# Kernel tuning notes

Measured on AMD Instinct MI355X. Metric: run time of the kernel, lower is better.

Reference implementation:

```python
import jax, jax.numpy as jnp
import numpy as np

EMBED_DIM = 768
NUM_HEADS = 12
EPS = 1e-6


def setup_inputs() -> dict:
    key = jax.random.key(0)
    ks = jax.random.split(key, 9)
    B, C, H, W = 8, EMBED_DIM, 48, 48
    std = 0.02
    E = EMBED_DIM
    return {
        "query": jax.random.normal(ks[0], (B, C, H, W), dtype=jnp.float32),
        "Wq": jax.random.normal(ks[1], (E, E), dtype=jnp.float32) * std,
        "bq": jnp.zeros((E,), dtype=jnp.float32),
        "Wk": jax.random.normal(ks[2], (E, E), dtype=jnp.float32) * std,
        "bk": jnp.zeros((E,), dtype=jnp.float32),
        "Wv": jax.random.normal(ks[3], (E, E), dtype=jnp.float32) * std,
        "bv": jnp.zeros((E,), dtype=jnp.float32),
        "Wo": jax.random.normal(ks[4], (E, E), dtype=jnp.float32) * std,
        "bo": jnp.zeros((E,), dtype=jnp.float32),
    }


def reference(query, Wq, bq, Wk, bk, Wv, bv, Wo, bo):
    # query: (B, C, H, W) -> (L, B, E) with L = H*W
    B, C, H, W = query.shape
    L = H * W
    E = C
    h = NUM_HEADS
    d = E // h
    x = query.reshape(B, C, L).transpose(2, 0, 1)  # (L, B, E)

    # cos/sin positional reweighting: pi/2 * (i+1) / L
    idx = (jnp.pi / 2) * jnp.arange(1, L + 1, dtype=x.dtype) / L
    sin = jnp.sin(idx)[None, :, None]  # (1, L, 1)
    cos = jnp.cos(idx)[None, :, None]

    # projections + relu feature map
    q = jax.nn.relu(x @ Wq.T + bq)
    k = jax.nn.relu(x @ Wk.T + bk)
    v = x @ Wv.T + bv

    def to_heads(t):  # (L, B, E) -> (B*h, L, d)
        return t.reshape(L, B * h, d).transpose(1, 0, 2)

    q, k, v = to_heads(q), to_heads(k), to_heads(v)

    q_ = jnp.concatenate([q * sin, q * cos], axis=-1)  # (n, L, 2d)
    k_ = jnp.concatenate([k * sin, k * cos], axis=-1)

    # non-causal linear attention
    kv = jnp.einsum("nld,nlm->ndm", k_, v)              # (n, 2d, d)
    z = 1.0 / jnp.maximum(jnp.einsum("nld,nd->nl", q_, k_.sum(axis=1)), EPS)
    out = jnp.einsum("nld,ndm,nl->nlm", q_, kv, z)       # (n, L, d)

    # residual (DropPath is identity at inference)
    attn = x + out.transpose(1, 0, 2).reshape(L, B, E)
    return attn @ Wo.T + bo
```

## Files before the change

### kernel.cpp

```cpp
#include <hip/hip_runtime.h>


#define L_SEQ 2304
#define BATCH 8
#define EDIM 768
#define NHEAD 12
#define DHEAD 64
#define MROWS (L_SEQ * BATCH)

typedef __attribute__((ext_vector_type(8))) short bf16x8_t;
typedef __attribute__((ext_vector_type(4))) float f32x4_t;

__device__ __forceinline__ float b2f(unsigned short u) {
  union { unsigned int i; float f; } x; x.i = ((unsigned int)u) << 16; return x.f;
}
__device__ __forceinline__ unsigned short f2b(float f) {
  union { float f; unsigned int i; } x; x.f = f;
  unsigned int r = x.i + 0x7FFFu + ((x.i >> 16) & 1u);
  return (unsigned short)(r >> 16);
}

#define GLOAD_LDS16(g, l)                                                     \
  __builtin_amdgcn_global_load_lds(                                           \
      (const __attribute__((address_space(1))) unsigned int*)(g),             \
      (__attribute__((address_space(3))) unsigned int*)(l), 16, 0, 0)

__global__ __launch_bounds__(256) void conv_w(
    const float* __restrict__ W0, const float* __restrict__ W1,
    const float* __restrict__ W2, const float* __restrict__ W3,
    unsigned short* __restrict__ dst) {
  const float* W = (blockIdx.y == 0) ? W0 : (blockIdx.y == 1) ? W1
                 : (blockIdx.y == 2) ? W2 : W3;
  unsigned short* d = dst + (size_t)blockIdx.y * EDIM * EDIM;
  int idx = blockIdx.x * 256 + threadIdx.x;
  float4 v = *(const float4*)(W + (size_t)idx * 4);
  ushort4 o;
  o.x = f2b(v.x); o.y = f2b(v.y); o.z = f2b(v.z); o.w = f2b(v.w);
  *(ushort4*)(d + (size_t)idx * 4) = o;
}

__global__ __launch_bounds__(256) void transpose_q(
    const float* __restrict__ q, unsigned short* __restrict__ xT) {
  __shared__ float tile[64][65];
  int b = blockIdx.z;
  int e0 = blockIdx.x * 64;
  int l0 = blockIdx.y * 64;
  int t = threadIdx.x;
  int li = t & 63, er = t >> 6;
#pragma unroll
  for (int p = 0; p < 16; p++) {
    int eo = er + p * 4;
    tile[eo][li] = q[((size_t)b * EDIM + (e0 + eo)) * L_SEQ + (l0 + li)];
  }
  __syncthreads();
  int ei = t & 63, lr = t >> 6;
#pragma unroll
  for (int p = 0; p < 16; p++) {
    int lo = lr + p * 4;
    xT[((size_t)b * L_SEQ + (l0 + lo)) * EDIM + (e0 + ei)] = f2b(tile[ei][lo]);
  }
}

template <int MODE>
__global__ __launch_bounds__(256) void gemm_bt(
    const unsigned short* __restrict__ A,
    const unsigned short* __restrict__ Wall,
    const float* __restrict__ bias0, const float* __restrict__ bias1,
    const float* __restrict__ bias2,
    unsigned short* __restrict__ dst0, unsigned short* __restrict__ dst1,
    unsigned short* __restrict__ dst2,
    float* __restrict__ dstf) {
  constexpr int BM = 128, BN = 128, BK = 32, K = EDIM;
  __shared__ __align__(16) unsigned short As[BM * BK];
  __shared__ __align__(16) unsigned short Bs[BN * BK];

  const unsigned short* W;
  const float* bias;
  unsigned short* dst;
  bool do_relu;
  if (MODE == 0) {
    int z = blockIdx.z;
    W    = Wall + (size_t)z * EDIM * EDIM;
    bias = (z == 0) ? bias0 : (z == 1) ? bias1 : bias2;
    dst  = (z == 0) ? dst0 : (z == 1) ? dst1 : dst2;
    do_relu = (z < 2);
  } else {
    W = Wall; bias = bias0; dst = dst0; do_relu = false;
  }

  int t = threadIdx.x;
  int lane = t & 63;
  int wave = t >> 6;
  int wr = (wave & 1) * 64;
  int wc = (wave >> 1) * 64;
  int row0 = blockIdx.x * BM;
  int col0 = blockIdx.y * BN;
  int mrow = lane & 15, quad = lane >> 4;

  f32x4_t acc[4][4] = {};

  for (int k0 = 0; k0 < K; k0 += BK) {
#pragma unroll
    for (int i = 0; i < 2; i++) {
      int c = t + i * 256;
      int r = c >> 2;
      int kk = (c & 3) * 8;
      GLOAD_LDS16(A + (size_t)(row0 + r) * K + (k0 + kk), As + (size_t)c * 8);
      GLOAD_LDS16(W + (size_t)(col0 + r) * K + (k0 + kk), Bs + (size_t)c * 8);
    }
    __syncthreads();
    bf16x8_t af[4], bfr[4];
#pragma unroll
    for (int i = 0; i < 4; i++) {
      af[i]  = *(const bf16x8_t*)(As + (wr + i * 16 + mrow) * BK + quad * 8);
      bfr[i] = *(const bf16x8_t*)(Bs + (wc + i * 16 + mrow) * BK + quad * 8);
    }
#pragma unroll
    for (int ti = 0; ti < 4; ti++)
#pragma unroll
      for (int tj = 0; tj < 4; tj++)
        acc[ti][tj] = __builtin_amdgcn_mfma_f32_16x16x32_bf16(af[ti], bfr[tj], acc[ti][tj], 0, 0, 0);
    __syncthreads();
  }

  int bb = row0 / L_SEQ;
#pragma unroll
  for (int ti = 0; ti < 4; ti++) {
#pragma unroll
    for (int tj = 0; tj < 4; tj++) {
      int gc = col0 + wc + tj * 16 + (lane & 15);
      float bv = bias[gc];
#pragma unroll
      for (int r = 0; r < 4; r++) {
        int gr = row0 + wr + ti * 16 + quad * 4 + r;
        float v = acc[ti][tj][r] + bv;
        if (MODE == 0) {
          if (do_relu) v = fmaxf(v, 0.0f);
          int ll = gr - bb * L_SEQ;
          int n = bb * NHEAD + (gc >> 6);
          dst[((size_t)n * L_SEQ + ll) * DHEAD + (gc & 63)] = f2b(v);
        } else {
          dstf[(size_t)gr * EDIM + gc] = v;
        }
      }
    }
  }
}

__global__ __launch_bounds__(256) void kv_mfma(
    const unsigned short* __restrict__ kbuf, const unsigned short* __restrict__ vbuf,
    float* __restrict__ kv, float* __restrict__ ksum) {
  constexpr int ST = 40;
  __shared__ __align__(16) unsigned short ksT[128 * ST];
  __shared__ __align__(16) unsigned short vsT[80 * ST];
  int n = blockIdx.x;
  int lbase = blockIdx.y * 288;
  int t = threadIdx.x;
  int lane = t & 63, wave = t >> 6;
  int mrow = lane & 15, quad = lane >> 4;

  for (int i = t; i < 16 * ST; i += 256) {
    int row = i / ST, col = i % ST;
    vsT[(64 + row) * ST + col] = (row == 0 && col < 32) ? (unsigned short)0x3F80 : 0;
  }

  int lrd = t >> 3;
  int oct = t & 7;
  const unsigned short* kbase = kbuf + (size_t)n * L_SEQ * DHEAD + oct * 8;
  const unsigned short* vbase = vbuf + (size_t)n * L_SEQ * DHEAD + oct * 8;

  f32x4_t acc[2][5] = {};

  for (int s = 0; s < 9; s++) {
    int l = lbase + s * 32 + lrd;
    float sv, cv;
    sincosf(1.5707963267948966f * (float)(l + 1) / 2304.0f, &sv, &cv);
    union { uint4 q; unsigned short u[8]; } kq, vq;
    kq.q = *(const uint4*)(kbase + (size_t)l * DHEAD);
    vq.q = *(const uint4*)(vbase + (size_t)l * DHEAD);
    __syncthreads();
#pragma unroll
    for (int e = 0; e < 8; e++) {
      int d = oct * 8 + e;
      float kval = b2f(kq.u[e]);
      ksT[d * ST + lrd] = f2b(kval * sv);
      ksT[(64 + d) * ST + lrd] = f2b(kval * cv);
      vsT[d * ST + lrd] = vq.u[e];
    }
    __syncthreads();
    bf16x8_t af[2];
#pragma unroll
    for (int ti = 0; ti < 2; ti++)
      af[ti] = *(const bf16x8_t*)(ksT + ((wave * 2 + ti) * 16 + mrow) * ST + quad * 8);
#pragma unroll
    for (int tj = 0; tj < 5; tj++) {
      bf16x8_t bfv = *(const bf16x8_t*)(vsT + (tj * 16 + mrow) * ST + quad * 8);
#pragma unroll
      for (int ti = 0; ti < 2; ti++)
        acc[ti][tj] = __builtin_amdgcn_mfma_f32_16x16x32_bf16(af[ti], bfv, acc[ti][tj], 0, 0, 0);
    }
  }

#pragma unroll
  for (int ti = 0; ti < 2; ti++) {
#pragma unroll
    for (int r = 0; r < 4; r++) {
      int j = (wave * 2 + ti) * 16 + quad * 4 + r;
#pragma unroll
      for (int tj = 0; tj < 4; tj++) {
        int m = tj * 16 + mrow;
        atomicAdd(&kv[((size_t)n * 128 + j) * 64 + m], acc[ti][tj][r]);
      }
      if (mrow == 0) atomicAdd(&ksum[n * 128 + j], acc[ti][4][r]);
    }
  }
}

__global__ __launch_bounds__(256) void attn_mfma(
    const unsigned short* __restrict__ qbuf, const float* __restrict__ kv,
    const float* __restrict__ ksum, const unsigned short* __restrict__ xT,
    unsigned short* __restrict__ attn) {
  __shared__ __align__(16) unsigned short As[128 * 72];
  __shared__ __align__(16) unsigned short Bs[64 * 136];
  __shared__ float ks_l[128];
  __shared__ float zs[128], zc[128];
  int l0 = blockIdx.x * 128;
  int n = blockIdx.y;
  int t = threadIdx.x;
  int lane = t & 63, wave = t >> 6;
  int mrow = lane & 15, quad = lane >> 4;
  int b = n / NHEAD, hd = n % NHEAD;

  {
    int row = t >> 1, off = (t & 1) * 32;
    const unsigned short* src = qbuf + ((size_t)n * L_SEQ + l0 + row) * DHEAD + off;
    unsigned short* d = As + row * 72 + off;
#pragma unroll
    for (int c = 0; c < 4; c++)
      *(uint4*)(d + c * 8) = *(const uint4*)(src + c * 8);
  }
  {
    int j = t >> 1, mh = (t & 1) * 32;
    const float* src = kv + ((size_t)n * 128 + j) * 64 + mh;
#pragma unroll
    for (int mm = 0; mm < 32; mm++)
      Bs[(mh + mm) * 136 + j] = f2b(src[mm]);
  }
  if (t < 128) ks_l[t] = ksum[n * 128 + t];
  __syncthreads();

  if (t < 128) {
    float d0 = 0.f, d1 = 0.f;
    const unsigned short* arow = As + t * 72;
#pragma unroll
    for (int j = 0; j < 8; j++) {
      bf16x8_t v = *(const bf16x8_t*)(arow + j * 8);
#pragma unroll
      for (int e = 0; e < 8; e++) {
        float qv = b2f((unsigned short)v[e]);
        d0 += qv * ks_l[j * 8 + e];
        d1 += qv * ks_l[64 + j * 8 + e];
      }
    }
    float sv, cv;
    sincosf(1.5707963267948966f * (float)(l0 + t + 1) / 2304.0f, &sv, &cv);
    float z = 1.0f / fmaxf(sv * d0 + cv * d1, 1e-6f);
    zs[t] = z * sv;
    zc[t] = z * cv;
  }
  __syncthreads();

  int wr = wave * 32;
  f32x4_t acc0[2][4] = {}, acc1[2][4] = {};
#pragma unroll
  for (int ks = 0; ks < 2; ks++) {
    bf16x8_t af[2];
#pragma unroll
    for (int ti = 0; ti < 2; ti++)
      af[ti] = *(const bf16x8_t*)(As + (wr + ti * 16 + mrow) * 72 + ks * 32 + quad * 8);
#pragma unroll
    for (int tj = 0; tj < 4; tj++) {
      bf16x8_t b0 = *(const bf16x8_t*)(Bs + (tj * 16 + mrow) * 136 + ks * 32 + quad * 8);
      bf16x8_t b1 = *(const bf16x8_t*)(Bs + (tj * 16 + mrow) * 136 + 64 + ks * 32 + quad * 8);
#pragma unroll
      for (int ti = 0; ti < 2; ti++) {
        acc0[ti][tj] = __builtin_amdgcn_mfma_f32_16x16x32_bf16(af[ti], b0, acc0[ti][tj], 0, 0, 0);
        acc1[ti][tj] = __builtin_amdgcn_mfma_f32_16x16x32_bf16(af[ti], b1, acc1[ti][tj], 0, 0, 0);
      }
    }
  }

#pragma unroll
  for (int ti = 0; ti < 2; ti++) {
#pragma unroll
    for (int tj = 0; tj < 4; tj++) {
      int m = tj * 16 + mrow;
#pragma unroll
      for (int r = 0; r < 4; r++) {
        int row = wr + ti * 16 + quad * 4 + r;
        int l = l0 + row;
        float ov = zs[row] * acc0[ti][tj][r] + zc[row] * acc1[ti][tj][r];
        float xv = b2f(xT[((size_t)b * L_SEQ + l) * EDIM + hd * DHEAD + m]);
        attn[((size_t)l * BATCH + b) * EDIM + hd * DHEAD + m] = f2b(xv + ov);
      }
    }
  }
}

extern "C" void kernel_launch(void* const* d_in, const int* in_sizes, int n_in,
                              void* d_out, int out_size, void* d_ws, size_t ws_size,
                              hipStream_t stream) {
  const float* query = (const float*)d_in[0];
  const float* Wq = (const float*)d_in[1];
  const float* bq = (const float*)d_in[2];
  const float* Wk = (const float*)d_in[3];
  const float* bk = (const float*)d_in[4];
  const float* Wv = (const float*)d_in[5];
  const float* bv = (const float*)d_in[6];
  const float* Wo = (const float*)d_in[7];
  const float* bo = (const float*)d_in[8];
  float* out = (float*)d_out;

  unsigned short* xT = (unsigned short*)d_out;

  char* ws = (char*)d_ws;
  const size_t SZ = (size_t)MROWS * EDIM * 2;
  unsigned short* qbuf = (unsigned short*)(ws);
  unsigned short* kbuf = (unsigned short*)(ws + SZ);
  unsigned short* vbuf = (unsigned short*)(ws + 2 * SZ);
  unsigned short* attn = kbuf;
  float* kv   = (float*)(ws + 3 * SZ);
  float* ksum = (float*)(ws + 3 * SZ + 3145728);
  unsigned short* wbf = (unsigned short*)(ws + 3 * SZ + 3145728 + 49152);

  conv_w<<<dim3(576, 4), 256, 0, stream>>>(Wq, Wk, Wv, Wo, wbf);

  transpose_q<<<dim3(12, 36, 8), 256, 0, stream>>>(query, xT);

  gemm_bt<0><<<dim3(MROWS / 128, EDIM / 128, 3), 256, 0, stream>>>(
      xT, wbf, bq, bk, bv, qbuf, kbuf, vbuf, nullptr);

  hipMemsetAsync(ws + 3 * SZ, 0, 3145728 + 49152, stream);

  kv_mfma<<<dim3(96, 8), 256, 0, stream>>>(kbuf, vbuf, kv, ksum);

  attn_mfma<<<dim3(L_SEQ / 128, 96), 256, 0, stream>>>(qbuf, kv, ksum, xT, attn);

  gemm_bt<1><<<dim3(MROWS / 128, EDIM / 128, 1), 256, 0, stream>>>(
      attn, wbf + 3 * (size_t)EDIM * EDIM, bo, nullptr, nullptr,
      nullptr, nullptr, nullptr, out);
}
```

Before: 329.7 us.

## Replace 128x128 GEMM with pipelined 256x256 tile kernel using swizzled LDS

Replaces the simple 128x128 single-buffered GEMM with a 256x256-tile, 512-thread kernel. It double-buffers K=64 tiles in 128KB of dynamic LDS and loads directly from global into LDS with an XOR swizzle to avoid bank conflicts. Loads are interleaved with MFMA quadrants using explicit barriers, waitcnts and setprio. It also remaps workgroup IDs for XCD-aware locality. The aim is to hide global-load latency and raise MFMA utilisation for the QKV and output projections. In exchange, the grid is much smaller (648 and 216 blocks) with heavier per-block register and LDS use, which limits occupancy and may cause tail effects.

```diff
diff --git a/kernel.cpp b/kernel.cpp
--- a/kernel.cpp
+++ b/kernel.cpp
@@ -61,8 +61,59 @@
   }
 }
 
+#define ALDSO(b_, h_) ((b_) * 16384 + (h_) * 8192)
+#define BLDSO(b_, h_) (32768 + (b_) * 16384 + (h_) * 8192)
+
+#define BARF()                                  \
+  {                                             \
+    asm volatile("" ::: "memory");              \
+    __builtin_amdgcn_s_barrier();               \
+    asm volatile("" ::: "memory");              \
+    __builtin_amdgcn_sched_barrier(0);          \
+  }
+#define WAITL()                                              \
+  {                                                          \
+    asm volatile("s_waitcnt lgkmcnt(0)" ::: "memory");       \
+    __builtin_amdgcn_sched_barrier(0);                       \
+  }
+#define VMW(N) asm volatile("s_waitcnt vmcnt(" #N ")" ::: "memory")
+
+#define STG_A(h_, kt_, LB_)                                                          \
+  {                                                                                  \
+    GLOAD_LDS16(a_sb + (size_t)((h_) * 128) * EDIM + (kt_) * 64, lds + (LB_) + t * 8); \
+    GLOAD_LDS16(a_sb + (size_t)((h_) * 128 + 64) * EDIM + (kt_) * 64,                \
+                lds + (LB_) + 4096 + t * 8);                                         \
+  }
+#define STG_B(h_, kt_, LB_)                                                          \
+  {                                                                                  \
+    GLOAD_LDS16(b_sb + (size_t)((h_) * 128) * EDIM + (kt_) * 64, lds + (LB_) + t * 8); \
+    GLOAD_LDS16(b_sb + (size_t)((h_) * 128 + 64) * EDIM + (kt_) * 64,                \
+                lds + (LB_) + 4096 + t * 8);                                         \
+  }
+
+#define DS_A(SET, B_, H_)                                                            \
+  _Pragma("unroll") for (int i_ = 0; i_ < 4; i_++)                                   \
+  _Pragma("unroll") for (int kk_ = 0; kk_ < 2; kk_++)                                \
+    SET[i_][kk_] = *(const bf16x8_t*)(lds + ALDSO(B_, H_) +                          \
+                                      ((a_base + i_ * 1024 + kk_ * 32) ^ xorv));
+
+#define DS_B(SET, B_, H_)                                                            \
+  _Pragma("unroll") for (int j_ = 0; j_ < 2; j_++)                                   \
+  _Pragma("unroll") for (int kk_ = 0; kk_ < 2; kk_++)                                \
+    SET[j_][kk_] = *(const bf16x8_t*)(lds + BLDSO(B_, H_) +                          \
+                                      ((b_base + j_ * 1024 + kk_ * 32) ^ xorv));
+
+#define MFMAQ(ASET, BSET, AH, BH)                                                    \
+  __builtin_amdgcn_s_setprio(1);                                                     \
+  _Pragma("unroll") for (int i_ = 0; i_ < 4; i_++)                                   \
+  _Pragma("unroll") for (int j_ = 0; j_ < 2; j_++)                                   \
+  _Pragma("unroll") for (int kk_ = 0; kk_ < 2; kk_++)                                \
+    acc[(AH) * 4 + i_][(BH) * 2 + j_] = __builtin_amdgcn_mfma_f32_16x16x32_bf16(     \
+        ASET[i_][kk_], BSET[j_][kk_], acc[(AH) * 4 + i_][(BH) * 2 + j_], 0, 0, 0);   \
+  __builtin_amdgcn_s_setprio(0);
+
 template <int MODE>
-__global__ __launch_bounds__(256) void gemm_bt(
+__global__ __launch_bounds__(512, 2) void gemm256(
     const unsigned short* __restrict__ A,
     const unsigned short* __restrict__ Wall,
     const float* __restrict__ bias0, const float* __restrict__ bias1,
@@ -70,69 +121,129 @@
     unsigned short* __restrict__ dst0, unsigned short* __restrict__ dst1,
     unsigned short* __restrict__ dst2,
     float* __restrict__ dstf) {
-  constexpr int BM = 128, BN = 128, BK = 32, K = EDIM;
-  __shared__ __align__(16) unsigned short As[BM * BK];
-  __shared__ __align__(16) unsigned short Bs[BN * BK];
+  extern __shared__ __align__(16) unsigned short lds[];
 
   const unsigned short* W;
   const float* bias;
-  unsigned short* dst;
-  bool do_relu;
-  if (MODE == 0) {
-    int z = blockIdx.z;
-    W    = Wall + (size_t)z * EDIM * EDIM;
-    bias = (z == 0) ? bias0 : (z == 1) ? bias1 : bias2;
-    dst  = (z == 0) ? dst0 : (z == 1) ? dst1 : dst2;
-    do_relu = (z < 2);
-  } else {
-    W = Wall; bias = bias0; dst = dst0; do_relu = false;
-  }
-
-  int t = threadIdx.x;
-  int lane = t & 63;
-  int wave = t >> 6;
-  int wr = (wave & 1) * 64;
-  int wc = (wave >> 1) * 64;
-  int row0 = blockIdx.x * BM;
-  int col0 = blockIdx.y * BN;
-  int mrow = lane & 15, quad = lane >> 4;
-
-  f32x4_t acc[4][4] = {};
-
-  for (int k0 = 0; k0 < K; k0 += BK) {
-#pragma unroll
-    for (int i = 0; i < 2; i++) {
-      int c = t + i * 256;
-      int r = c >> 2;
-      int kk = (c & 3) * 8;
-      GLOAD_LDS16(A + (size_t)(row0 + r) * K + (k0 + kk), As + (size_t)c * 8);
-      GLOAD_LDS16(W + (size_t)(col0 + r) * K + (k0 + kk), Bs + (size_t)c * 8);
-    }
-    __syncthreads();
-    bf16x8_t af[4], bfr[4];
-#pragma unroll
-    for (int i = 0; i < 4; i++) {
-      af[i]  = *(const bf16x8_t*)(As + (wr + i * 16 + mrow) * BK + quad * 8);
-      bfr[i] = *(const bf16x8_t*)(Bs + (wc + i * 16 + mrow) * BK + quad * 8);
-    }
-#pragma unroll
-    for (int ti = 0; ti < 4; ti++)
-#pragma unroll
-      for (int tj = 0; tj < 4; tj++)
-        acc[ti][tj] = __builtin_amdgcn_mfma_f32_16x16x32_bf16(af[ti], bfr[tj], acc[ti][tj], 0, 0, 0);
-    __syncthreads();
-  }
-
-  int bb = row0 / L_SEQ;
-#pragma unroll
-  for (int ti = 0; ti < 4; ti++) {
+  unsigned short* dst = nullptr;
+  bool do_relu = false;
+  int rowblk, colblk;
+  {
+    int nwg = (int)gridDim.x;
+    int wg = ((int)blockIdx.x & 7) * (nwg >> 3) + ((int)blockIdx.x >> 3);
+    if (MODE == 0) {
+      rowblk = wg / 9;
+      int c = wg - rowblk * 9;
+      colblk = c % 3;
+      int z = c / 3;
+      W = Wall + (size_t)z * EDIM * EDIM;
+      bias = (z == 0) ? bias0 : (z == 1) ? bias1 : bias2;
+      dst = (z == 0) ? dst0 : (z == 1) ? dst1 : dst2;
+      do_relu = (z < 2);
+    } else {
+      rowblk = wg / 3;
+      colblk = wg - rowblk * 3;
+      W = Wall;
+      bias = bias0;
+    }
+  }
+  const int row0 = rowblk * 256;
+  const int col0 = colblk * 256;
+
+  const int t = threadIdx.x;
+  const int lane = t & 63;
+  const int wave = t >> 6;
+  const int wm = wave >> 2;
+  const int wn = wave & 3;
+  const int mrow = lane & 15;
+  const int quad = lane >> 4;
+
+  const int xorv = (mrow & 7) << 3;
+  const int a_base = (wm * 64 + mrow) * 64 + quad * 8;
+  const int b_base = (wn * 32 + mrow) * 64 + quad * 8;
+
+  const int lr_s = t >> 3;
+  const int k0_s = ((((t >> 3) & 7) ^ (t & 7)) << 3);
+  const unsigned short* a_sb = A + (size_t)(row0 + lr_s) * EDIM + k0_s;
+  const unsigned short* b_sb = W + (size_t)(col0 + lr_s) * EDIM + k0_s;
+
+  f32x4_t acc[8][4] = {};
+  bf16x8_t aA[4][2], aB[4][2], bA[2][2], bB[2][2];
+
+  STG_A(0, 0, ALDSO(0, 0));
+  STG_B(0, 0, BLDSO(0, 0));
+  STG_A(1, 0, ALDSO(0, 1));
+  STG_B(1, 0, BLDSO(0, 1));
+  STG_A(0, 1, ALDSO(1, 0));
+  STG_B(0, 1, BLDSO(1, 0));
+  VMW(4);
+  BARF();
+
+#pragma unroll
+  for (int i = 0; i < 6; ++i) {
+    const int kt0 = 2 * i, kt1 = 2 * i + 1;
+    const bool nxt = (i < 5);
+    DS_A(aA, 0, 0);
+    DS_B(bA, 0, 0);
+    STG_A(1, kt1, ALDSO(1, 1));
+    BARF();
+    WAITL();
+    MFMAQ(aA, bA, 0, 0);
+    BARF();
+    DS_B(bB, 0, 1);
+    STG_B(1, kt1, BLDSO(1, 1));
+    BARF();
+    WAITL();
+    MFMAQ(aA, bB, 0, 1);
+    BARF();
+    DS_A(aB, 0, 1);
+    if (nxt) STG_A(0, kt0 + 2, ALDSO(0, 0));
+    BARF();
+    WAITL();
+    MFMAQ(aB, bA, 1, 0);
+    BARF();
+    if (nxt) STG_B(0, kt0 + 2, BLDSO(0, 0));
+    BARF();
+    MFMAQ(aB, bB, 1, 1);
+    if (nxt) { VMW(4); } else { VMW(0); }
+    BARF();
+    DS_A(aA, 1, 0);
+    DS_B(bA, 1, 0);
+    if (nxt) STG_A(1, kt0 + 2, ALDSO(0, 1));
+    BARF();
+    WAITL();
+    MFMAQ(aA, bA, 0, 0);
+    BARF();
+    DS_B(bB, 1, 1);
+    if (nxt) STG_B(1, kt0 + 2, BLDSO(0, 1));
+    BARF();
+    WAITL();
+    MFMAQ(aA, bB, 0, 1);
+    BARF();
+    DS_A(aB, 1, 1);
+    if (nxt) STG_A(0, kt1 + 2, ALDSO(1, 0));
+    BARF();
+    WAITL();
+    MFMAQ(aB, bA, 1, 0);
+    BARF();
+    if (nxt) STG_B(0, kt1 + 2, BLDSO(1, 0));
+    BARF();
+    MFMAQ(aB, bB, 1, 1);
+    if (nxt) { VMW(4); } else { VMW(0); }
+    BARF();
+  }
+
+  const int bb = row0 / L_SEQ;
+#pragma unroll
+  for (int ti = 0; ti < 8; ti++) {
+    int rbase = row0 + (ti >> 2) * 128 + wm * 64 + (ti & 3) * 16 + quad * 4;
 #pragma unroll
     for (int tj = 0; tj < 4; tj++) {
-      int gc = col0 + wc + tj * 16 + (lane & 15);
+      int gc = col0 + (tj >> 1) * 128 + wn * 32 + (tj & 1) * 16 + mrow;
       float bv = bias[gc];
 #pragma unroll
       for (int r = 0; r < 4; r++) {
-        int gr = row0 + wr + ti * 16 + quad * 4 + r;
+        int gr = rbase + r;
         float v = acc[ti][tj][r] + bv;
         if (MODE == 0) {
           if (do_relu) v = fmaxf(v, 0.0f);
@@ -333,11 +444,20 @@
   float* ksum = (float*)(ws + 3 * SZ + 3145728);
   unsigned short* wbf = (unsigned short*)(ws + 3 * SZ + 3145728 + 49152);
 
+  static bool attr_done = false;
+  if (!attr_done) {
+    (void)hipFuncSetAttribute((const void*)gemm256<0>,
+                              hipFuncAttributeMaxDynamicSharedMemorySize, 131072);
+    (void)hipFuncSetAttribute((const void*)gemm256<1>,
+                              hipFuncAttributeMaxDynamicSharedMemorySize, 131072);
+    attr_done = true;
+  }
+
   conv_w<<<dim3(576, 4), 256, 0, stream>>>(Wq, Wk, Wv, Wo, wbf);
 
   transpose_q<<<dim3(12, 36, 8), 256, 0, stream>>>(query, xT);
 
-  gemm_bt<0><<<dim3(MROWS / 128, EDIM / 128, 3), 256, 0, stream>>>(
+  gemm256<0><<<dim3(648), dim3(512), 131072, stream>>>(
       xT, wbf, bq, bk, bv, qbuf, kbuf, vbuf, nullptr);
 
   hipMemsetAsync(ws + 3 * SZ, 0, 3145728 + 49152, stream);
@@ -346,7 +466,7 @@
 
   attn_mfma<<<dim3(L_SEQ / 128, 96), 256, 0, stream>>>(qbuf, kv, ksum, xT, attn);
 
-  gemm_bt<1><<<dim3(MROWS / 128, EDIM / 128, 1), 256, 0, stream>>>(
+  gemm256<1><<<dim3(216), dim3(512), 131072, stream>>>(
       attn, wbf + 3 * (size_t)EDIM * EDIM, bo, nullptr, nullptr,
       nullptr, nullptr, nullptr, out);
 }
```

After: 297.0 us. -9.9%, faster.
